# Performance work log

Measured on AMD Instinct MI355X. Metric: run time of the kernel, lower is better.

## Reference

```python
import jax, jax.numpy as jnp
import numpy as np

K_NN = 4  # hard-coded k in get_graph_feature(x, k=4)


def _conv1(h, Wm, s, b):
    # 1x1 conv1d + folded-BN (scale/shift) + ReLU
    return jax.nn.relu(jnp.einsum('oc,bcn->bon', Wm, h) * s[:, None] + b[:, None])


def _conv2(h, Wm, s, b):
    # 1x1 conv2d + folded-BN + ReLU
    return jax.nn.relu(jnp.einsum('oc,bcnk->bonk', Wm, h) * s[:, None, None] + b[:, None, None])


def _forward(x, W_dup, s_dup, b_dup, W_c1, s_c1, b_c1,
             W2a, s2a, b2a, W2b, s2b, b2b, W2c, s2c, b2c,
             W3a, s3a, b3a, W3b, s3b, b3b, W4a, bias4a, W4b, bias4b):
    B = x.shape[0]
    h = _conv1(x, W_dup, s_dup, b_dup)           # (B,256,1024)
    h = h.reshape(B, 128, 2048)                  # duplicate points: (B,128,2048)
    h = _conv1(h, W_c1, s_c1, b_c1)              # (B,64,2048)
    g = jnp.max(h, axis=2, keepdims=True)        # max_pool1d over all 2048 -> (B,64,1)
    # knn on 64-d features: pairwise = -||xi-xj||^2, topk picks nearest (self included)
    xx = jnp.sum(h * h, axis=1, keepdims=True)   # (B,1,P)
    inner = -2.0 * jnp.einsum('bcn,bcm->bnm', h, h)
    pd = -xx - inner - jnp.swapaxes(xx, 1, 2)    # (B,P,P)
    idx = jax.lax.top_k(pd, K_NN)[1]             # (B,P,k)
    xt = jnp.swapaxes(h, 1, 2)                   # (B,P,C)
    nb = xt[jnp.arange(B)[:, None, None], idx]   # gather neighbors: (B,P,k,C)
    ctr = xt[:, :, None, :]
    feat = jnp.concatenate([nb - ctr, jnp.broadcast_to(ctr, nb.shape)], axis=-1)  # (B,P,k,2C)
    feat = jnp.transpose(feat, (0, 3, 1, 2))     # (B,128,P,k)
    feat = _conv2(feat, W2a, s2a, b2a)
    feat = _conv2(feat, W2b, s2b, b2b)
    feat = _conv2(feat, W2c, s2c, b2c)           # (B,64,P,k)
    local = jnp.max(feat, axis=3)                # max over k -> (B,64,P)
    g = _conv1(g, W3a, s3a, b3a)
    g = _conv1(g, W3b, s3b, b3b)                 # (B,128,1)
    final = jnp.concatenate([local, jnp.broadcast_to(g, (B, 128, local.shape[2]))], axis=1)  # (B,192,P)
    h4 = jax.nn.relu(jnp.einsum('oc,bcn->bon', W4a, final) + bias4a[:, None])  # (B,256,P)
    out = jnp.einsum('oc,bcn->bon', W4b, h4) + bias4b[:, None]                 # (B,3,P)
    return out


def setup_inputs() -> dict:
    key = jax.random.key(0)
    ks = list(jax.random.split(key, 30))
    W = lambda k, o, c: jax.random.normal(k, (o, c), jnp.float32) * 0.05
    sc = lambda k, c: 1.0 + 0.1 * jax.random.normal(k, (c,), jnp.float32)
    bs = lambda k, c: 0.1 * jax.random.normal(k, (c,), jnp.float32)
    return {
        'search_keypoint': jax.random.normal(ks[0], (8, 128, 1024), jnp.float32),
        'W_dup': W(ks[1], 256, 128), 's_dup': sc(ks[2], 256), 'b_dup': bs(ks[3], 256),
        'W_c1': W(ks[4], 64, 128), 's_c1': sc(ks[5], 64), 'b_c1': bs(ks[6], 64),
        'W2a': W(ks[7], 64, 128), 's2a': sc(ks[8], 64), 'b2a': bs(ks[9], 64),
        'W2b': W(ks[10], 64, 64), 's2b': sc(ks[11], 64), 'b2b': bs(ks[12], 64),
        'W2c': W(ks[13], 64, 64), 's2c': sc(ks[14], 64), 'b2c': bs(ks[15], 64),
        'W3a': W(ks[16], 128, 64), 's3a': sc(ks[17], 128), 'b3a': bs(ks[18], 128),
        'W3b': W(ks[19], 128, 128), 's3b': sc(ks[20], 128), 'b3b': bs(ks[21], 128),
        'W4a': W(ks[22], 256, 192), 'bias4a': bs(ks[23], 256),
        'W4b': W(ks[24], 3, 256), 'bias4b': bs(ks[25], 3),
    }


def reference(search_keypoint, W_dup, s_dup, b_dup, W_c1, s_c1, b_c1,
              W2a, s2a, b2a, W2b, s2b, b2b, W2c, s2c, b2c,
              W3a, s3a, b3a, W3b, s3b, b3b, W4a, bias4a, W4b, bias4b):
    return _forward(search_keypoint, W_dup, s_dup, b_dup, W_c1, s_c1, b_c1,
                    W2a, s2a, b2a, W2b, s2b, b2b, W2c, s2c, b2c,
                    W3a, s3a, b3a, W3b, s3b, b3b, W4a, bias4a, W4b, bias4b)
```

## Files before the change

### kernel.cpp

```cpp
#include <hip/hip_runtime.h>
#include <float.h>

typedef __attribute__((ext_vector_type(8))) short short8;
typedef __attribute__((ext_vector_type(4))) float f32x4;
typedef unsigned short u16;
typedef unsigned long long u64;

static constexpr size_t OFF_W     = 0;
static constexpr size_t OFF_YZ    = 131072;
static constexpr size_t OFF_Zf    = 1179648;
static constexpr size_t OFF_FEATR = 2228224;
static constexpr size_t OFF_FIN   = 6422528;
static constexpr size_t OFF_XX    = 9568256;
static constexpr size_t OFF_G     = 9584640;
static constexpr size_t OFF_G4    = 9617408;
static constexpr size_t WS_FLOATS = 9652736;

static constexpr size_t WO_DUP = 0;
static constexpr size_t WO_C1  = 32768;
static constexpr size_t WO_2A  = 40960;
static constexpr size_t WO_2B  = 49152;
static constexpr size_t WO_2C  = 53248;
static constexpr size_t WO_4A  = 57344;

__device__ __forceinline__ void gl_lds16(const void* g, void* l) {
    __builtin_amdgcn_global_load_lds(
        (const __attribute__((address_space(1))) void*)g,
        (__attribute__((address_space(3))) void*)l, 16, 0, 0);
}

__device__ __forceinline__ u16 f2bf(float x) {
    union { float f; unsigned int u; } v; v.f = x;
    unsigned int r = v.u + 0x7fffu + ((v.u >> 16) & 1u);
    return (u16)(r >> 16);
}
__device__ __forceinline__ float bf2f(u16 h) {
    union { unsigned int u; float f; } v; v.u = ((unsigned int)h) << 16;
    return v.f;
}
__device__ __forceinline__ void split2(float x, u16& h, u16& l) {
    h = f2bf(x);
    l = f2bf(x - bf2f(h));
}

__device__ __forceinline__ unsigned int fmap(float f) {
    unsigned int u = __float_as_uint(f);
    return u ^ ((unsigned int)((int)u >> 31) | 0x80000000u);
}
__device__ __forceinline__ u64 mkkey(float f, int m) {
    return ((u64)fmap(f) << 32) | (unsigned int)(2047 - m);
}
static __device__ __forceinline__ void ins4k(u64 k, u64 bk[4])
{
#pragma unroll
    for (int s = 0; s < 4; ++s) {
        bool better = k > bk[s];
        u64 t = bk[s];
        bk[s] = better ? k : bk[s];
        k = better ? t : k;
    }
}

__global__ __launch_bounds__(256) void prep(
    const float* __restrict__ W_dup, const float* __restrict__ W_c1,
    const float* __restrict__ W2a, const float* __restrict__ W2b,
    const float* __restrict__ W2c, const float* __restrict__ W4a,
    const float* __restrict__ x,
    u16* __restrict__ whi, u16* __restrict__ wlo,
    u16* __restrict__ xthi, u16* __restrict__ xtlo)
{
    __shared__ float tile[64][65];
    if (blockIdx.x < 416) {
        int t = blockIdx.x * 256 + threadIdx.x;
        float v;
        if      (t < 40960) v = (t < 32768) ? W_dup[t] : W_c1[t - 32768];
        else if (t < 53248) v = (t < 49152) ? W2a[t - 40960] : W2b[t - 49152];
        else                v = (t < 57344) ? W2c[t - 53248] : W4a[t - 57344];
        u16 h, l; split2(v, h, l);
        whi[t] = h; wlo[t] = l;
    } else {
        const int bb = blockIdx.x - 416;
        const int n0 = (bb & 15) * 64;
        const int c0 = ((bb >> 4) & 1) * 64;
        const int b  = bb >> 5;
        const int t  = threadIdx.x;
        const float* xb = x + ((size_t)b * 128 + c0) * 1024;
#pragma unroll
        for (int i = 0; i < 16; ++i) {
            int c = i * 4 + (t >> 6), n = t & 63;
            tile[c][n] = xb[(size_t)c * 1024 + n0 + n];
        }
        __syncthreads();
#pragma unroll
        for (int i = 0; i < 16; ++i) {
            int n = i * 4 + (t >> 6), c = t & 63;
            u16 h, l; split2(tile[c][n], h, l);
            const size_t o = ((size_t)b * 1024 + n0 + n) * 128 + c0 + c;
            xthi[o] = h; xtlo[o] = l;
        }
    }
}

__global__ __launch_bounds__(512) void backbone(
    const u16* __restrict__ xthi, const u16* __restrict__ xtlo,
    const u16* __restrict__ whi, const u16* __restrict__ wlo,
    const float* __restrict__ s_dup, const float* __restrict__ b_dup,
    const float* __restrict__ s_c1, const float* __restrict__ b_c1,
    u16* __restrict__ h2thi, u16* __restrict__ h2tlo,
    float* __restrict__ xxb, float* __restrict__ gp,
    float* __restrict__ y, float* __restrict__ z)
{
    const int t = threadIdx.x;
    const int wu = t >> 6;
    const int lane = t & 63;
    const int j = lane & 15, q = lane >> 4;
    const int nb = blockIdx.x;
    const int b  = blockIdx.y;
    const int n0 = nb * 16;

    __shared__ __align__(16) u16 h1h[32 * 136], h1l[32 * 136];
    __shared__ __align__(16) u16 h2h[32 * 72],  h2l[32 * 72];
    __shared__ float xxp[2][4][16];
    __shared__ float gpart[2][64];

    {
        const size_t arow = ((size_t)b * 1024 + n0 + j) * 128;
        short8 ahv[4], alv[4];
#pragma unroll
        for (int ks = 0; ks < 4; ++ks) {
            ahv[ks] = *(const short8*)(xthi + arow + q * 8 + ks * 32);
            alv[ks] = *(const short8*)(xtlo + arow + q * 8 + ks * 32);
        }
        const u16* wdh = whi + WO_DUP;
        const u16* wdl = wlo + WO_DUP;
#pragma unroll
        for (int ci = 0; ci < 2; ++ci) {
            const int ctile = wu * 2 + ci;
            const int o = ctile * 16 + j;
            f32x4 acc = (f32x4){0.f, 0.f, 0.f, 0.f};
#pragma unroll
            for (int ks = 0; ks < 4; ++ks) {
                short8 bh = *(const short8*)(wdh + (size_t)o * 128 + q * 8 + ks * 32);
                short8 bl = *(const short8*)(wdl + (size_t)o * 128 + q * 8 + ks * 32);
                acc = __builtin_amdgcn_mfma_f32_16x16x32_bf16(ahv[ks], bh, acc, 0, 0, 0);
                acc = __builtin_amdgcn_mfma_f32_16x16x32_bf16(ahv[ks], bl, acc, 0, 0, 0);
                acc = __builtin_amdgcn_mfma_f32_16x16x32_bf16(alv[ks], bh, acc, 0, 0, 0);
            }
            const float sc = s_dup[o], bi = b_dup[o];
            const int lrbase = (j & 1) * 16;
            const int col = ctile * 8 + (j >> 1);
#pragma unroll
            for (int r = 0; r < 4; ++r) {
                float v = fmaxf(acc[r] * sc + bi, 0.f);
                u16 h, l; split2(v, h, l);
                const int lr = lrbase + q * 4 + r;
                h1h[lr * 136 + col] = h;
                h1l[lr * 136 + col] = l;
            }
        }
    }
    __syncthreads();

    {
        const int g = wu >> 2, cq = wu & 3;
        short8 ahv[4], alv[4];
#pragma unroll
        for (int ks = 0; ks < 4; ++ks) {
            ahv[ks] = *(const short8*)&h1h[(g * 16 + j) * 136 + q * 8 + ks * 32];
            alv[ks] = *(const short8*)&h1l[(g * 16 + j) * 136 + q * 8 + ks * 32];
        }
        const u16* wch = whi + WO_C1;
        const u16* wcl = wlo + WO_C1;
        const int o = cq * 16 + j;
        f32x4 acc = (f32x4){0.f, 0.f, 0.f, 0.f};
#pragma unroll
        for (int ks = 0; ks < 4; ++ks) {
            short8 bh = *(const short8*)(wch + (size_t)o * 128 + q * 8 + ks * 32);
            short8 bl = *(const short8*)(wcl + (size_t)o * 128 + q * 8 + ks * 32);
            acc = __builtin_amdgcn_mfma_f32_16x16x32_bf16(ahv[ks], bh, acc, 0, 0, 0);
            acc = __builtin_amdgcn_mfma_f32_16x16x32_bf16(ahv[ks], bl, acc, 0, 0, 0);
            acc = __builtin_amdgcn_mfma_f32_16x16x32_bf16(alv[ks], bh, acc, 0, 0, 0);
        }
        const float sc = s_c1[o], bi = b_c1[o];
        float sq[4];
        float cm = -FLT_MAX;
#pragma unroll
        for (int r = 0; r < 4; ++r) {
            float v = fmaxf(acc[r] * sc + bi, 0.f);
            sq[r] = v * v;
            cm = fmaxf(cm, v);
            u16 h, l; split2(v, h, l);
            const size_t R = (size_t)b * 2048 + g * 1024 + n0 + q * 4 + r;
            h2thi[R * 64 + o] = h;
            h2tlo[R * 64 + o] = l;
            const int lr = g * 16 + q * 4 + r;
            h2h[lr * 72 + o] = h;
            h2l[lr * 72 + o] = l;
        }
#pragma unroll
        for (int r = 0; r < 4; ++r) {
#pragma unroll
            for (int mask = 1; mask < 16; mask <<= 1)
                sq[r] += __shfl_xor(sq[r], mask, 64);
        }
        if (j == 0) {
#pragma unroll
            for (int r = 0; r < 4; ++r) xxp[g][cq][q * 4 + r] = sq[r];
        }
        cm = fmaxf(cm, __shfl_xor(cm, 16, 64));
        cm = fmaxf(cm, __shfl_xor(cm, 32, 64));
        if (q == 0) gpart[g][cq * 16 + j] = cm;
    }
    __syncthreads();

    if (t < 32) {
        const int g = t >> 4, i = t & 15;
        xxb[(size_t)b * 2048 + g * 1024 + n0 + i] =
            (xxp[g][0][i] + xxp[g][1][i]) + (xxp[g][2][i] + xxp[g][3][i]);
    }
    if (t >= 64 && t < 128) {
        const int c = t - 64;
        gp[((size_t)b * 64 + nb) * 64 + c] = fmaxf(gpart[0][c], gpart[1][c]);
    }

    {
        const int g = wu >> 2, half = (wu >> 1) & 1, cg = wu & 1;
        short8 ahv[2], alv[2];
#pragma unroll
        for (int ks = 0; ks < 2; ++ks) {
            ahv[ks] = *(const short8*)&h2h[(g * 16 + j) * 72 + q * 8 + ks * 32];
            alv[ks] = *(const short8*)&h2l[(g * 16 + j) * 72 + q * 8 + ks * 32];
        }
        const u16* w2h = whi + WO_2A;
        const u16* w2l = wlo + WO_2A;
        float* dst = half ? z : y;
#pragma unroll
        for (int ci = 0; ci < 2; ++ci) {
            const int o = (cg * 2 + ci) * 16 + j;
            f32x4 acc = (f32x4){0.f, 0.f, 0.f, 0.f};
#pragma unroll
            for (int ks = 0; ks < 2; ++ks) {
                short8 bh = *(const short8*)(w2h + (size_t)o * 128 + half * 64 + q * 8 + ks * 32);
                short8 bl = *(const short8*)(w2l + (size_t)o * 128 + half * 64 + q * 8 + ks * 32);
                acc = __builtin_amdgcn_mfma_f32_16x16x32_bf16(ahv[ks], bh, acc, 0, 0, 0);
                acc = __builtin_amdgcn_mfma_f32_16x16x32_bf16(ahv[ks], bl, acc, 0, 0, 0);
                acc = __builtin_amdgcn_mfma_f32_16x16x32_bf16(alv[ks], bh, acc, 0, 0, 0);
            }
#pragma unroll
            for (int r = 0; r < 4; ++r) {
                const size_t R = (size_t)b * 2048 + g * 1024 + n0 + q * 4 + r;
                dst[R * 64 + o] = acc[r];
            }
        }
    }
}

struct __align__(16) KBuf {
    u16 hi[4096];
    u16 lo[4096];
    float xm[64];
};

__global__ __launch_bounds__(256) void knn_topk(const u16* __restrict__ thi,
                                                const u16* __restrict__ tlo,
                                                const float* __restrict__ xx,
                                                u64* __restrict__ part)
{
    const int b    = blockIdx.z;
    const int mh   = blockIdx.y;
    const int t    = threadIdx.x;
    const int wu   = __builtin_amdgcn_readfirstlane(t >> 6);
    const int lane = t & 63;
    const int j    = lane & 15;
    const int q    = lane >> 4;
    const int nrow0 = blockIdx.x * 64 + wu * 16;

    const u16* th = thi + (size_t)b * 2048 * 64;
    const u16* tl = tlo + (size_t)b * 2048 * 64;
    const float* xb = xx + (size_t)b * 2048;

    __shared__ KBuf sb[2];

    const size_t arow = (size_t)(nrow0 + j) * 64;
    short8 ah0 = *(const short8*)(th + arow + q * 8);
    short8 ah1 = *(const short8*)(th + arow + 32 + q * 8);
    short8 al0 = *(const short8*)(tl + arow + q * 8);
    short8 al1 = *(const short8*)(tl + arow + 32 + q * 8);

    u64 bk[4][4];
#pragma unroll
    for (int r = 0; r < 4; ++r)
#pragma unroll
        for (int s = 0; s < 4; ++s) bk[r][s] = 0ull;

    const int mbeg = mh * 1024;

#define KNN_STAGE(BUF, M0)                                                        \
    {                                                                             \
        const u16* sh = th + (size_t)((M0) + lane) * 64;                          \
        const u16* sl = tl + (size_t)((M0) + lane) * 64;                          \
        gl_lds16(sh + (2 * wu) * 8,     &sb[BUF].hi[(2 * wu) * 512]);             \
        gl_lds16(sh + (2 * wu + 1) * 8, &sb[BUF].hi[(2 * wu + 1) * 512]);         \
        gl_lds16(sl + (2 * wu) * 8,     &sb[BUF].lo[(2 * wu) * 512]);             \
        gl_lds16(sl + (2 * wu + 1) * 8, &sb[BUF].lo[(2 * wu + 1) * 512]);         \
        if (wu == 0 && lane < 16) gl_lds16(xb + (M0) + lane * 4, &sb[BUF].xm[0]); \
    }

    KNN_STAGE(0, mbeg)

    for (int tt = 0; tt < 16; ++tt) {
        __syncthreads();
        if (tt < 15) KNN_STAGE((tt + 1) & 1, mbeg + (tt + 1) * 64)
        const KBuf& bf = sb[tt & 1];
        const int m0 = mbeg + tt * 64;

        float pds[4][4];
#pragma unroll
        for (int sub = 0; sub < 4; ++sub) {
            const int ml = sub * 16 + j;
            short8 bh0 = *(const short8*)&bf.hi[(q) * 512 + ml * 8];
            short8 bh1 = *(const short8*)&bf.hi[(4 + q) * 512 + ml * 8];
            short8 bl0 = *(const short8*)&bf.lo[(q) * 512 + ml * 8];
            short8 bl1 = *(const short8*)&bf.lo[(4 + q) * 512 + ml * 8];
            const float xmv = bf.xm[ml];
            f32x4 accA = (f32x4){0.f, 0.f, 0.f, 0.f};
            f32x4 accB = (f32x4){0.f, 0.f, 0.f, 0.f};
            accA = __builtin_amdgcn_mfma_f32_16x16x32_bf16(ah0, bh0, accA, 0, 0, 0);
            accB = __builtin_amdgcn_mfma_f32_16x16x32_bf16(ah1, bh1, accB, 0, 0, 0);
            accA = __builtin_amdgcn_mfma_f32_16x16x32_bf16(ah0, bl0, accA, 0, 0, 0);
            accB = __builtin_amdgcn_mfma_f32_16x16x32_bf16(ah1, bl1, accB, 0, 0, 0);
            accA = __builtin_amdgcn_mfma_f32_16x16x32_bf16(al0, bh0, accA, 0, 0, 0);
            accB = __builtin_amdgcn_mfma_f32_16x16x32_bf16(al1, bh1, accB, 0, 0, 0);
            accA = __builtin_amdgcn_mfma_f32_16x16x32_bf16(al0, bl0, accA, 0, 0, 0);
            accB = __builtin_amdgcn_mfma_f32_16x16x32_bf16(al1, bl1, accB, 0, 0, 0);
#pragma unroll
            for (int r = 0; r < 4; ++r)
                pds[sub][r] = __builtin_fmaf(2.f, accA[r] + accB[r], -xmv);
        }

#pragma unroll
        for (int r = 0; r < 4; ++r) {
            float mx = fmaxf(fmaxf(pds[0][r], pds[1][r]), fmaxf(pds[2][r], pds[3][r]));
            if (fmap(mx) >= (unsigned int)(bk[r][3] >> 32)) {
#pragma unroll
                for (int sub = 0; sub < 4; ++sub) {
                    u64 key = mkkey(pds[sub][r], m0 + sub * 16 + j);
                    if (key > bk[r][3]) ins4k(key, bk[r]);
                }
            }
        }
    }
#undef KNN_STAGE

#pragma unroll
    for (int rr = 0; rr < 4; ++rr) {
#pragma unroll
        for (int mask = 1; mask < 16; mask <<= 1) {
            u64 pk[4];
#pragma unroll
            for (int s = 0; s < 4; ++s) pk[s] = __shfl_xor(bk[rr][s], mask, 64);
#pragma unroll
            for (int s = 0; s < 4; ++s) ins4k(pk[s], bk[rr]);
        }
    }
    if (j == 0) {
#pragma unroll
        for (int r = 0; r < 4; ++r) {
            const int nrow = nrow0 + q * 4 + r;
            u64* pp = part + (((size_t)b * 2 + mh) * 2048 + nrow) * 4;
            pp[0] = bk[r][0]; pp[1] = bk[r][1]; pp[2] = bk[r][2]; pp[3] = bk[r][3];
        }
    }
}

__global__ __launch_bounds__(128) void gconv_kernel(
    const float* __restrict__ gp,
    const float* __restrict__ W3a, const float* __restrict__ s3a, const float* __restrict__ b3a,
    const float* __restrict__ W3b, const float* __restrict__ s3b, const float* __restrict__ b3b,
    const float* __restrict__ W4a, float* __restrict__ g4)
{
    const int b = blockIdx.x;
    const int t = threadIdx.x;
    __shared__ float gl[64], ga[128], gb[128];
    if (t < 64) {
        float m = -FLT_MAX;
        for (int s = 0; s < 64; ++s)
            m = fmaxf(m, gp[((size_t)b * 64 + s) * 64 + t]);
        gl[t] = m;
    }
    __syncthreads();
    float a = 0.f;
#pragma unroll
    for (int c = 0; c < 64; ++c) a += W3a[t * 64 + c] * gl[c];
    ga[t] = fmaxf(a * s3a[t] + b3a[t], 0.f);
    __syncthreads();
    float o = 0.f;
#pragma unroll
    for (int c = 0; c < 128; ++c) o += W3b[t * 128 + c] * ga[c];
    gb[t] = fmaxf(o * s3b[t] + b3b[t], 0.f);
    __syncthreads();
    for (int oo = t; oo < 256; oo += 128) {
        float s = 0.f;
#pragma unroll 4
        for (int c = 0; c < 128; ++c)
            s += W4a[(size_t)oo * 192 + 64 + c] * gb[c];
        g4[(size_t)b * 256 + oo] = s;
    }
}

__global__ __launch_bounds__(64) void fused_edge(
    const u64* __restrict__ part,
    const float* __restrict__ y, const float* __restrict__ z,
    const float* __restrict__ s2a, const float* __restrict__ b2a,
    const u16* __restrict__ w2bh, const u16* __restrict__ w2bl,
    const float* __restrict__ s2b, const float* __restrict__ b2b,
    const u16* __restrict__ w2ch, const u16* __restrict__ w2cl,
    const float* __restrict__ s2c, const float* __restrict__ b2c,
    u16* __restrict__ finhi, u16* __restrict__ finlo)
{
    const int lane = threadIdx.x & 63;
    const int j = lane & 15, q = lane >> 4;
    const int gb = blockIdx.x;
    const int b = gb >> 9;
    const int n0 = (gb & 511) * 4;

    __shared__ __align__(16) u16 plh[16 * 72];
    __shared__ __align__(16) u16 pll[16 * 72];
    __shared__ int sidx[16];

    if (lane < 4) {
        const int n = n0 + lane;
        u64 fk[4] = {0ull, 0ull, 0ull, 0ull};
#pragma unroll
        for (int qt = 0; qt < 2; ++qt) {
            const u64* pp = part + (((size_t)b * 2 + qt) * 2048 + n) * 4;
#pragma unroll
            for (int s = 0; s < 4; ++s) ins4k(pp[s], fk);
        }
        int4 ii;
        ii.x = 2047 - (int)(fk[0] & 0x7ff);
        ii.y = 2047 - (int)(fk[1] & 0x7ff);
        ii.z = 2047 - (int)(fk[2] & 0x7ff);
        ii.w = 2047 - (int)(fk[3] & 0x7ff);
        *(int4*)&sidx[lane * 4] = ii;
    }

    {
        const int row = lane >> 2;
        const int c0 = (lane & 3) * 16;
        const int id = sidx[row];
        const int nfull = n0 + (row >> 2);
        const float* yb = y + (size_t)b * 2048 * 64;
        const float* yi = yb + (size_t)id * 64;
        const float* yn = yb + (size_t)nfull * 64;
        const float* zn = z + ((size_t)b * 2048 + nfull) * 64;
        u16* oh = &plh[row * 72 + c0];
        u16* ol = &pll[row * 72 + c0];
#pragma unroll
        for (int cc = 0; cc < 16; cc += 4) {
            const int c = c0 + cc;
            float4 a  = *(const float4*)(yi + c);
            float4 bq = *(const float4*)(yn + c);
            float4 cq = *(const float4*)(zn + c);
            float4 sv = *(const float4*)(s2a + c);
            float4 bb = *(const float4*)(b2a + c);
            float v0 = fmaxf((a.x - bq.x + cq.x) * sv.x + bb.x, 0.f);
            float v1 = fmaxf((a.y - bq.y + cq.y) * sv.y + bb.y, 0.f);
            float v2 = fmaxf((a.z - bq.z + cq.z) * sv.z + bb.z, 0.f);
            float v3 = fmaxf((a.w - bq.w + cq.w) * sv.w + bb.w, 0.f);
            union { u16 u[4]; uint2 v; } ph, pl;
            split2(v0, ph.u[0], pl.u[0]);
            split2(v1, ph.u[1], pl.u[1]);
            split2(v2, ph.u[2], pl.u[2]);
            split2(v3, ph.u[3], pl.u[3]);
            *(uint2*)(oh + cc) = ph.v;
            *(uint2*)(ol + cc) = pl.v;
        }
    }

    {
        const int abase = j * 72 + q * 8;
        short8 ah0 = *(const short8*)&plh[abase];
        short8 ah1 = *(const short8*)&plh[abase + 32];
        short8 al0 = *(const short8*)&pll[abase];
        short8 al1 = *(const short8*)&pll[abase + 32];
#pragma unroll
        for (int ct = 0; ct < 4; ++ct) {
            const int o = ct * 16 + j;
            short8 bh0 = *(const short8*)(w2bh + (size_t)o * 64 + q * 8);
            short8 bh1 = *(const short8*)(w2bh + (size_t)o * 64 + 32 + q * 8);
            short8 bl0 = *(const short8*)(w2bl + (size_t)o * 64 + q * 8);
            short8 bl1 = *(const short8*)(w2bl + (size_t)o * 64 + 32 + q * 8);
            f32x4 acc = (f32x4){0.f, 0.f, 0.f, 0.f};
            acc = __builtin_amdgcn_mfma_f32_16x16x32_bf16(ah0, bh0, acc, 0, 0, 0);
            acc = __builtin_amdgcn_mfma_f32_16x16x32_bf16(ah0, bl0, acc, 0, 0, 0);
            acc = __builtin_amdgcn_mfma_f32_16x16x32_bf16(al0, bh0, acc, 0, 0, 0);
            acc = __builtin_amdgcn_mfma_f32_16x16x32_bf16(ah1, bh1, acc, 0, 0, 0);
            acc = __builtin_amdgcn_mfma_f32_16x16x32_bf16(ah1, bl1, acc, 0, 0, 0);
            acc = __builtin_amdgcn_mfma_f32_16x16x32_bf16(al1, bh1, acc, 0, 0, 0);
            const float sc = s2b[o], bi = b2b[o];
#pragma unroll
            for (int r = 0; r < 4; ++r) {
                float v = fmaxf(acc[r] * sc + bi, 0.f);
                u16 h, l; split2(v, h, l);
                const int row = q * 4 + r;
                plh[row * 72 + o] = h;
                pll[row * 72 + o] = l;
            }
        }
    }

    {
        const int abase = j * 72 + q * 8;
        short8 ah0 = *(const short8*)&plh[abase];
        short8 ah1 = *(const short8*)&plh[abase + 32];
        short8 al0 = *(const short8*)&pll[abase];
        short8 al1 = *(const short8*)&pll[abase + 32];
        const size_t finrow = (size_t)b * 2048 + n0 + q;
#pragma unroll
        for (int ct = 0; ct < 4; ++ct) {
            const int o = ct * 16 + j;
            short8 bh0 = *(const short8*)(w2ch + (size_t)o * 64 + q * 8);
            short8 bh1 = *(const short8*)(w2ch + (size_t)o * 64 + 32 + q * 8);
            short8 bl0 = *(const short8*)(w2cl + (size_t)o * 64 + q * 8);
            short8 bl1 = *(const short8*)(w2cl + (size_t)o * 64 + 32 + q * 8);
            f32x4 acc = (f32x4){0.f, 0.f, 0.f, 0.f};
            acc = __builtin_amdgcn_mfma_f32_16x16x32_bf16(ah0, bh0, acc, 0, 0, 0);
            acc = __builtin_amdgcn_mfma_f32_16x16x32_bf16(ah0, bl0, acc, 0, 0, 0);
            acc = __builtin_amdgcn_mfma_f32_16x16x32_bf16(al0, bh0, acc, 0, 0, 0);
            acc = __builtin_amdgcn_mfma_f32_16x16x32_bf16(ah1, bh1, acc, 0, 0, 0);
            acc = __builtin_amdgcn_mfma_f32_16x16x32_bf16(ah1, bl1, acc, 0, 0, 0);
            acc = __builtin_amdgcn_mfma_f32_16x16x32_bf16(al1, bh1, acc, 0, 0, 0);
            const float sc = s2c[o], bi = b2c[o];
            float m = -FLT_MAX;
#pragma unroll
            for (int r = 0; r < 4; ++r)
                m = fmaxf(m, fmaxf(acc[r] * sc + bi, 0.f));
            u16 h, l; split2(m, h, l);
            finhi[finrow * 64 + o] = h;
            finlo[finrow * 64 + o] = l;
        }
    }
}

__global__ __launch_bounds__(64) void conv_final(
    const u16* __restrict__ Whi, const u16* __restrict__ Wlo,
    const float* __restrict__ bias,
    const u16* __restrict__ Ahi, const u16* __restrict__ Alo,
    const float* __restrict__ g4,
    const float* __restrict__ W2, const float* __restrict__ bias2,
    float* __restrict__ out)
{
    const int lane = threadIdx.x & 63;
    const int j = lane & 15, q = lane >> 4;
    const int n0g = blockIdx.x * 16;
    const int b = n0g >> 11;

    short8 a_hi[2], a_lo[2];
    const u16* arow_h = Ahi + (size_t)(n0g + j) * 64 + q * 8;
    const u16* arow_l = Alo + (size_t)(n0g + j) * 64 + q * 8;
#pragma unroll
    for (int ks = 0; ks < 2; ++ks) {
        a_hi[ks] = *(const short8*)(arow_h + ks * 32);
        a_lo[ks] = *(const short8*)(arow_l + ks * 32);
    }

    float p[3][4];
#pragma unroll
    for (int oo = 0; oo < 3; ++oo)
#pragma unroll
        for (int r = 0; r < 4; ++r) p[oo][r] = 0.f;

#pragma unroll
    for (int ct = 0; ct < 16; ++ct) {
        const int o = ct * 16 + j;
        const u16* wr_h = Whi + (size_t)o * 192 + q * 8;
        const u16* wr_l = Wlo + (size_t)o * 192 + q * 8;
        f32x4 acc = (f32x4){0.f, 0.f, 0.f, 0.f};
#pragma unroll
        for (int ks = 0; ks < 2; ++ks) {
            short8 bh = *(const short8*)(wr_h + ks * 32);
            short8 bl = *(const short8*)(wr_l + ks * 32);
            acc = __builtin_amdgcn_mfma_f32_16x16x32_bf16(a_hi[ks], bh, acc, 0, 0, 0);
            acc = __builtin_amdgcn_mfma_f32_16x16x32_bf16(a_hi[ks], bl, acc, 0, 0, 0);
            acc = __builtin_amdgcn_mfma_f32_16x16x32_bf16(a_lo[ks], bh, acc, 0, 0, 0);
        }
        const float bi = bias[o] + g4[(size_t)b * 256 + o];
        float w0 = W2[o], w1 = W2[256 + o], w2 = W2[512 + o];
#pragma unroll
        for (int r = 0; r < 4; ++r) {
            float v = fmaxf(acc[r] + bi, 0.f);
            p[0][r] += w0 * v;
            p[1][r] += w1 * v;
            p[2][r] += w2 * v;
        }
    }

#pragma unroll
    for (int oo = 0; oo < 3; ++oo)
#pragma unroll
        for (int r = 0; r < 4; ++r) {
#pragma unroll
            for (int mask = 1; mask < 16; mask <<= 1)
                p[oo][r] += __shfl_xor(p[oo][r], mask, 64);
        }
    if (j == 0) {
        const int row0 = n0g + q * 4;
#pragma unroll
        for (int r = 0; r < 4; ++r) {
            const int n = (row0 + r) & 2047;
#pragma unroll
            for (int oo = 0; oo < 3; ++oo)
                out[((size_t)b * 3 + oo) * 2048 + n] = p[oo][r] + bias2[oo];
        }
    }
}

extern "C" void kernel_launch(void* const* d_in, const int* in_sizes, int n_in,
                              void* d_out, int out_size, void* d_ws, size_t ws_size,
                              hipStream_t stream)
{
    const float* x     = (const float*)d_in[0];
    const float* W_dup = (const float*)d_in[1];
    const float* s_dup = (const float*)d_in[2];
    const float* b_dup = (const float*)d_in[3];
    const float* W_c1  = (const float*)d_in[4];
    const float* s_c1  = (const float*)d_in[5];
    const float* b_c1  = (const float*)d_in[6];
    const float* W2a   = (const float*)d_in[7];
    const float* s2a   = (const float*)d_in[8];
    const float* b2a   = (const float*)d_in[9];
    const float* W2b   = (const float*)d_in[10];
    const float* s2b   = (const float*)d_in[11];
    const float* b2b   = (const float*)d_in[12];
    const float* W2c   = (const float*)d_in[13];
    const float* s2c   = (const float*)d_in[14];
    const float* b2c   = (const float*)d_in[15];
    const float* W3a   = (const float*)d_in[16];
    const float* s3a   = (const float*)d_in[17];
    const float* b3a   = (const float*)d_in[18];
    const float* W3b   = (const float*)d_in[19];
    const float* s3b   = (const float*)d_in[20];
    const float* b3b   = (const float*)d_in[21];
    const float* W4a   = (const float*)d_in[22];
    const float* b4a   = (const float*)d_in[23];
    const float* W4b   = (const float*)d_in[24];
    const float* b4b   = (const float*)d_in[25];

    if (ws_size < WS_FLOATS * sizeof(float)) return;

    float* ws = (float*)d_ws;
    u16* whi   = (u16*)(ws + OFF_W);
    u16* wlo   = whi + 131072;
    u16* xthi  = (u16*)(ws + OFF_FEATR);
    u16* xtlo  = xthi + 1048576;
    u64* part  = (u64*)(ws + OFF_FEATR);
    float* y    = ws + OFF_YZ;
    float* z    = ws + OFF_Zf;
    u16* h2thi = (u16*)(ws + OFF_FIN);
    u16* h2tlo = h2thi + 1048576;
    u16* finhi  = (u16*)(ws + OFF_FIN);
    u16* finlo  = finhi + 1048576;
    float* xxb  = ws + OFF_XX;
    float* gp   = ws + OFF_G;
    float* g4   = ws + OFF_G4;
    float* out  = (float*)d_out;

    prep<<<672, 256, 0, stream>>>(W_dup, W_c1, W2a, W2b, W2c, W4a, x,
                                  whi, wlo, xthi, xtlo);
    backbone<<<dim3(64, 8), 512, 0, stream>>>(
        xthi, xtlo, whi, wlo, s_dup, b_dup, s_c1, b_c1,
        h2thi, h2tlo, xxb, gp, y, z);
    gconv_kernel<<<8, 128, 0, stream>>>(gp, W3a, s3a, b3a, W3b, s3b, b3b, W4a, g4);
    knn_topk<<<dim3(32, 2, 8), 256, 0, stream>>>(h2thi, h2tlo, xxb, part);
    fused_edge<<<4096, 64, 0, stream>>>(
        part, y, z, s2a, b2a,
        whi + WO_2B, wlo + WO_2B, s2b, b2b,
        whi + WO_2C, wlo + WO_2C, s2c, b2c,
        finhi, finlo);
    conv_final<<<1024, 64, 0, stream>>>(
        whi + WO_4A, wlo + WO_4A, b4a, finhi, finlo, g4, W4b, b4b, out);
}
```

Measured before the change: 244.7 us.

## Fuse final conv into edge kernel and shrink kNN tiles to 32 candidates

```diff
diff --git a/kernel.cpp b/kernel.cpp
--- a/kernel.cpp
+++ b/kernel.cpp
@@ -256,12 +256,12 @@
 }
 
 struct __align__(16) KBuf {
-    u16 hi[4096];
-    u16 lo[4096];
-    float xm[64];
+    u16 hi[2048];
+    u16 lo[2048];
+    float xm[32];
 };
 
-__global__ __launch_bounds__(256) void knn_topk(const u16* __restrict__ thi,
+__global__ __launch_bounds__(128) void knn_topk(const u16* __restrict__ thi,
                                                 const u16* __restrict__ tlo,
                                                 const float* __restrict__ xx,
                                                 u64* __restrict__ part)
@@ -273,7 +273,7 @@
     const int lane = t & 63;
     const int j    = lane & 15;
     const int q    = lane >> 4;
-    const int nrow0 = blockIdx.x * 64 + wu * 16;
+    const int nrow0 = blockIdx.x * 32 + wu * 16;
 
     const u16* th = thi + (size_t)b * 2048 * 64;
     const u16* tl = tlo + (size_t)b * 2048 * 64;
@@ -297,31 +297,32 @@
 
 #define KNN_STAGE(BUF, M0)                                                        \
     {                                                                             \
-        const u16* sh = th + (size_t)((M0) + lane) * 64;                          \
-        const u16* sl = tl + (size_t)((M0) + lane) * 64;                          \
-        gl_lds16(sh + (2 * wu) * 8,     &sb[BUF].hi[(2 * wu) * 512]);             \
-        gl_lds16(sh + (2 * wu + 1) * 8, &sb[BUF].hi[(2 * wu + 1) * 512]);         \
-        gl_lds16(sl + (2 * wu) * 8,     &sb[BUF].lo[(2 * wu) * 512]);             \
-        gl_lds16(sl + (2 * wu + 1) * 8, &sb[BUF].lo[(2 * wu + 1) * 512]);         \
-        if (wu == 0 && lane < 16) gl_lds16(xb + (M0) + lane * 4, &sb[BUF].xm[0]); \
+        _Pragma("unroll")                                                         \
+        for (int ii = 0; ii < 2; ++ii) {                                          \
+            const int s = (wu * 2 + ii) * 64 + lane;                              \
+            const int ml = s & 31, ch = s >> 5;                                   \
+            gl_lds16(th + (size_t)((M0) + ml) * 64 + ch * 8, &sb[BUF].hi[s * 8]); \
+            gl_lds16(tl + (size_t)((M0) + ml) * 64 + ch * 8, &sb[BUF].lo[s * 8]); \
+        }                                                                         \
+        if (wu == 0 && lane < 8) gl_lds16(xb + (M0) + lane * 4, &sb[BUF].xm[0]);  \
     }
 
     KNN_STAGE(0, mbeg)
 
-    for (int tt = 0; tt < 16; ++tt) {
+    for (int tt = 0; tt < 32; ++tt) {
         __syncthreads();
-        if (tt < 15) KNN_STAGE((tt + 1) & 1, mbeg + (tt + 1) * 64)
+        if (tt < 31) KNN_STAGE((tt + 1) & 1, mbeg + (tt + 1) * 32)
         const KBuf& bf = sb[tt & 1];
-        const int m0 = mbeg + tt * 64;
-
-        float pds[4][4];
-#pragma unroll
-        for (int sub = 0; sub < 4; ++sub) {
+        const int m0 = mbeg + tt * 32;
+
+        float pds[2][4];
+#pragma unroll
+        for (int sub = 0; sub < 2; ++sub) {
             const int ml = sub * 16 + j;
-            short8 bh0 = *(const short8*)&bf.hi[(q) * 512 + ml * 8];
-            short8 bh1 = *(const short8*)&bf.hi[(4 + q) * 512 + ml * 8];
-            short8 bl0 = *(const short8*)&bf.lo[(q) * 512 + ml * 8];
-            short8 bl1 = *(const short8*)&bf.lo[(4 + q) * 512 + ml * 8];
+            short8 bh0 = *(const short8*)&bf.hi[(q * 32 + ml) * 8];
+            short8 bh1 = *(const short8*)&bf.hi[((4 + q) * 32 + ml) * 8];
+            short8 bl0 = *(const short8*)&bf.lo[(q * 32 + ml) * 8];
+            short8 bl1 = *(const short8*)&bf.lo[((4 + q) * 32 + ml) * 8];
             const float xmv = bf.xm[ml];
             f32x4 accA = (f32x4){0.f, 0.f, 0.f, 0.f};
             f32x4 accB = (f32x4){0.f, 0.f, 0.f, 0.f};
@@ -340,10 +341,10 @@
 
 #pragma unroll
         for (int r = 0; r < 4; ++r) {
-            float mx = fmaxf(fmaxf(pds[0][r], pds[1][r]), fmaxf(pds[2][r], pds[3][r]));
+            float mx = fmaxf(pds[0][r], pds[1][r]);
             if (fmap(mx) >= (unsigned int)(bk[r][3] >> 32)) {
 #pragma unroll
-                for (int sub = 0; sub < 4; ++sub) {
+                for (int sub = 0; sub < 2; ++sub) {
                     u64 key = mkkey(pds[sub][r], m0 + sub * 16 + j);
                     if (key > bk[r][3]) ins4k(key, bk[r]);
                 }
@@ -408,7 +409,7 @@
     }
 }
 
-__global__ __launch_bounds__(64) void fused_edge(
+__global__ __launch_bounds__(256) void fused_edge(
     const u64* __restrict__ part,
     const float* __restrict__ y, const float* __restrict__ z,
     const float* __restrict__ s2a, const float* __restrict__ b2a,
@@ -416,20 +417,28 @@
     const float* __restrict__ s2b, const float* __restrict__ b2b,
     const u16* __restrict__ w2ch, const u16* __restrict__ w2cl,
     const float* __restrict__ s2c, const float* __restrict__ b2c,
-    u16* __restrict__ finhi, u16* __restrict__ finlo)
+    const u16* __restrict__ w4ah, const u16* __restrict__ w4al,
+    const float* __restrict__ b4a, const float* __restrict__ g4,
+    const float* __restrict__ W4b, const float* __restrict__ b4b,
+    float* __restrict__ out)
 {
-    const int lane = threadIdx.x & 63;
+    const int t = threadIdx.x;
+    const int wu = t >> 6;
+    const int lane = t & 63;
     const int j = lane & 15, q = lane >> 4;
-    const int gb = blockIdx.x;
-    const int b = gb >> 9;
-    const int n0 = (gb & 511) * 4;
-
-    __shared__ __align__(16) u16 plh[16 * 72];
-    __shared__ __align__(16) u16 pll[16 * 72];
-    __shared__ int sidx[16];
+    const int b = blockIdx.x >> 7;
+    const int n0 = (blockIdx.x & 127) * 16;
+    const int nw0 = n0 + wu * 4;
+
+    __shared__ __align__(16) u16 plh[64 * 72];
+    __shared__ __align__(16) u16 pll[64 * 72];
+    __shared__ __align__(16) u16 finh[16 * 72];
+    __shared__ __align__(16) u16 finl[16 * 72];
+    __shared__ float pred[4][3][16];
+    __shared__ int sidx[64];
 
     if (lane < 4) {
-        const int n = n0 + lane;
+        const int n = nw0 + lane;
         u64 fk[4] = {0ull, 0ull, 0ull, 0ull};
 #pragma unroll
         for (int qt = 0; qt < 2; ++qt) {
@@ -442,20 +451,20 @@
         ii.y = 2047 - (int)(fk[1] & 0x7ff);
         ii.z = 2047 - (int)(fk[2] & 0x7ff);
         ii.w = 2047 - (int)(fk[3] & 0x7ff);
-        *(int4*)&sidx[lane * 4] = ii;
+        *(int4*)&sidx[wu * 16 + lane * 4] = ii;
     }
 
     {
         const int row = lane >> 2;
         const int c0 = (lane & 3) * 16;
-        const int id = sidx[row];
-        const int nfull = n0 + (row >> 2);
+        const int id = sidx[wu * 16 + row];
+        const int nfull = nw0 + (row >> 2);
         const float* yb = y + (size_t)b * 2048 * 64;
         const float* yi = yb + (size_t)id * 64;
         const float* yn = yb + (size_t)nfull * 64;
         const float* zn = z + ((size_t)b * 2048 + nfull) * 64;
-        u16* oh = &plh[row * 72 + c0];
-        u16* ol = &pll[row * 72 + c0];
+        u16* oh = &plh[(wu * 16 + row) * 72 + c0];
+        u16* ol = &pll[(wu * 16 + row) * 72 + c0];
 #pragma unroll
         for (int cc = 0; cc < 16; cc += 4) {
             const int c = c0 + cc;
@@ -479,7 +488,7 @@
     }
 
     {
-        const int abase = j * 72 + q * 8;
+        const int abase = (wu * 16 + j) * 72 + q * 8;
         short8 ah0 = *(const short8*)&plh[abase];
         short8 ah1 = *(const short8*)&plh[abase + 32];
         short8 al0 = *(const short8*)&pll[abase];
@@ -503,7 +512,7 @@
             for (int r = 0; r < 4; ++r) {
                 float v = fmaxf(acc[r] * sc + bi, 0.f);
                 u16 h, l; split2(v, h, l);
-                const int row = q * 4 + r;
+                const int row = wu * 16 + q * 4 + r;
                 plh[row * 72 + o] = h;
                 pll[row * 72 + o] = l;
             }
@@ -511,12 +520,11 @@
     }
 
     {
-        const int abase = j * 72 + q * 8;
+        const int abase = (wu * 16 + j) * 72 + q * 8;
         short8 ah0 = *(const short8*)&plh[abase];
         short8 ah1 = *(const short8*)&plh[abase + 32];
         short8 al0 = *(const short8*)&pll[abase];
         short8 al1 = *(const short8*)&pll[abase + 32];
-        const size_t finrow = (size_t)b * 2048 + n0 + q;
 #pragma unroll
         for (int ct = 0; ct < 4; ++ct) {
             const int o = ct * 16 + j;
@@ -537,82 +545,73 @@
             for (int r = 0; r < 4; ++r)
                 m = fmaxf(m, fmaxf(acc[r] * sc + bi, 0.f));
             u16 h, l; split2(m, h, l);
-            finhi[finrow * 64 + o] = h;
-            finlo[finrow * 64 + o] = l;
-        }
-    }
-}
-
-__global__ __launch_bounds__(64) void conv_final(
-    const u16* __restrict__ Whi, const u16* __restrict__ Wlo,
-    const float* __restrict__ bias,
-    const u16* __restrict__ Ahi, const u16* __restrict__ Alo,
-    const float* __restrict__ g4,
-    const float* __restrict__ W2, const float* __restrict__ bias2,
-    float* __restrict__ out)
-{
-    const int lane = threadIdx.x & 63;
-    const int j = lane & 15, q = lane >> 4;
-    const int n0g = blockIdx.x * 16;
-    const int b = n0g >> 11;
-
-    short8 a_hi[2], a_lo[2];
-    const u16* arow_h = Ahi + (size_t)(n0g + j) * 64 + q * 8;
-    const u16* arow_l = Alo + (size_t)(n0g + j) * 64 + q * 8;
-#pragma unroll
-    for (int ks = 0; ks < 2; ++ks) {
-        a_hi[ks] = *(const short8*)(arow_h + ks * 32);
-        a_lo[ks] = *(const short8*)(arow_l + ks * 32);
-    }
-
-    float p[3][4];
-#pragma unroll
-    for (int oo = 0; oo < 3; ++oo)
-#pragma unroll
-        for (int r = 0; r < 4; ++r) p[oo][r] = 0.f;
-
-#pragma unroll
-    for (int ct = 0; ct < 16; ++ct) {
-        const int o = ct * 16 + j;
-        const u16* wr_h = Whi + (size_t)o * 192 + q * 8;
-        const u16* wr_l = Wlo + (size_t)o * 192 + q * 8;
-        f32x4 acc = (f32x4){0.f, 0.f, 0.f, 0.f};
+            const int frow = wu * 4 + q;
+            finh[frow * 72 + o] = h;
+            finl[frow * 72 + o] = l;
+        }
+    }
+    __syncthreads();
+
+    {
+        short8 a_hi[2], a_lo[2];
 #pragma unroll
         for (int ks = 0; ks < 2; ++ks) {
-            short8 bh = *(const short8*)(wr_h + ks * 32);
-            short8 bl = *(const short8*)(wr_l + ks * 32);
-            acc = __builtin_amdgcn_mfma_f32_16x16x32_bf16(a_hi[ks], bh, acc, 0, 0, 0);
-            acc = __builtin_amdgcn_mfma_f32_16x16x32_bf16(a_hi[ks], bl, acc, 0, 0, 0);
-            acc = __builtin_amdgcn_mfma_f32_16x16x32_bf16(a_lo[ks], bh, acc, 0, 0, 0);
-        }
-        const float bi = bias[o] + g4[(size_t)b * 256 + o];
-        float w0 = W2[o], w1 = W2[256 + o], w2 = W2[512 + o];
-#pragma unroll
-        for (int r = 0; r < 4; ++r) {
-            float v = fmaxf(acc[r] + bi, 0.f);
-            p[0][r] += w0 * v;
-            p[1][r] += w1 * v;
-            p[2][r] += w2 * v;
-        }
-    }
-
-#pragma unroll
-    for (int oo = 0; oo < 3; ++oo)
-#pragma unroll
-        for (int r = 0; r < 4; ++r) {
-#pragma unroll
-            for (int mask = 1; mask < 16; mask <<= 1)
-                p[oo][r] += __shfl_xor(p[oo][r], mask, 64);
-        }
-    if (j == 0) {
-        const int row0 = n0g + q * 4;
-#pragma unroll
-        for (int r = 0; r < 4; ++r) {
-            const int n = (row0 + r) & 2047;
+            a_hi[ks] = *(const short8*)&finh[j * 72 + q * 8 + ks * 32];
+            a_lo[ks] = *(const short8*)&finl[j * 72 + q * 8 + ks * 32];
+        }
+        float p[3][4];
+#pragma unroll
+        for (int oo = 0; oo < 3; ++oo)
+#pragma unroll
+            for (int r = 0; r < 4; ++r) p[oo][r] = 0.f;
+
+#pragma unroll
+        for (int ci = 0; ci < 4; ++ci) {
+            const int o = (wu * 4 + ci) * 16 + j;
+            const u16* wr_h = w4ah + (size_t)o * 192 + q * 8;
+            const u16* wr_l = w4al + (size_t)o * 192 + q * 8;
+            f32x4 acc = (f32x4){0.f, 0.f, 0.f, 0.f};
+#pragma unroll
+            for (int ks = 0; ks < 2; ++ks) {
+                short8 bh = *(const short8*)(wr_h + ks * 32);
+                short8 bl = *(const short8*)(wr_l + ks * 32);
+                acc = __builtin_amdgcn_mfma_f32_16x16x32_bf16(a_hi[ks], bh, acc, 0, 0, 0);
+                acc = __builtin_amdgcn_mfma_f32_16x16x32_bf16(a_hi[ks], bl, acc, 0, 0, 0);
+                acc = __builtin_amdgcn_mfma_f32_16x16x32_bf16(a_lo[ks], bh, acc, 0, 0, 0);
+            }
+            const float bi = b4a[o] + g4[(size_t)b * 256 + o];
+            float w0 = W4b[o], w1 = W4b[256 + o], w2 = W4b[512 + o];
+#pragma unroll
+            for (int r = 0; r < 4; ++r) {
+                float v = fmaxf(acc[r] + bi, 0.f);
+                p[0][r] += w0 * v;
+                p[1][r] += w1 * v;
+                p[2][r] += w2 * v;
+            }
+        }
+#pragma unroll
+        for (int oo = 0; oo < 3; ++oo)
+#pragma unroll
+            for (int r = 0; r < 4; ++r) {
+#pragma unroll
+                for (int mask = 1; mask < 16; mask <<= 1)
+                    p[oo][r] += __shfl_xor(p[oo][r], mask, 64);
+            }
+        if (j == 0) {
 #pragma unroll
             for (int oo = 0; oo < 3; ++oo)
-                out[((size_t)b * 3 + oo) * 2048 + n] = p[oo][r] + bias2[oo];
-        }
+#pragma unroll
+                for (int r = 0; r < 4; ++r)
+                    pred[wu][oo][q * 4 + r] = p[oo][r];
+        }
+    }
+    __syncthreads();
+
+    if (t < 48) {
+        const int oo = t >> 4, rr = t & 15;
+        float s = (pred[0][oo][rr] + pred[1][oo][rr]) +
+                  (pred[2][oo][rr] + pred[3][oo][rr]) + b4b[oo];
+        out[((size_t)b * 3 + oo) * 2048 + n0 + rr] = s;
     }
 }
 
@@ -659,8 +658,6 @@
     float* z    = ws + OFF_Zf;
     u16* h2thi = (u16*)(ws + OFF_FIN);
     u16* h2tlo = h2thi + 1048576;
-    u16* finhi  = (u16*)(ws + OFF_FIN);
-    u16* finlo  = finhi + 1048576;
     float* xxb  = ws + OFF_XX;
     float* gp   = ws + OFF_G;
     float* g4   = ws + OFF_G4;
@@ -672,12 +669,10 @@
         xthi, xtlo, whi, wlo, s_dup, b_dup, s_c1, b_c1,
         h2thi, h2tlo, xxb, gp, y, z);
     gconv_kernel<<<8, 128, 0, stream>>>(gp, W3a, s3a, b3a, W3b, s3b, b3b, W4a, g4);
-    knn_topk<<<dim3(32, 2, 8), 256, 0, stream>>>(h2thi, h2tlo, xxb, part);
-    fused_edge<<<4096, 64, 0, stream>>>(
+    knn_topk<<<dim3(64, 2, 8), 128, 0, stream>>>(h2thi, h2tlo, xxb, part);
+    fused_edge<<<1024, 256, 0, stream>>>(
         part, y, z, s2a, b2a,
         whi + WO_2B, wlo + WO_2B, s2b, b2b,
         whi + WO_2C, wlo + WO_2C, s2c, b2c,
-        finhi, finlo);
-    conv_final<<<1024, 64, 0, stream>>>(
-        whi + WO_4A, wlo + WO_4A, b4a, finhi, finlo, g4, W4b, b4b, out);
-}
+        whi + WO_4A, wlo + WO_4A, b4a, g4, W4b, b4b, out);
+}
```

After: 246.3 us. Within noise of the previous version (+0.7%).
